# Performance work log

Hardware: AMD Instinct MI355X
Metric: run time of the kernel (lower is better)

## Reference

```python
import jax, jax.numpy as jnp
import numpy as np

B, N, F, F1 = 1024, 75, 512, 256
NEG = -1.0e9
ALPHA = 0.2  # LeakyReLU slope


def setup_inputs() -> dict:
    key = jax.random.key(0)
    k1, k2, k3, k4 = jax.random.split(key, 4)
    X = jax.random.normal(k1, (B, N, F), dtype=jnp.float32)
    A = jax.random.randint(k2, (N, N), 0, 2, dtype=jnp.int32)  # binary adjacency
    W = jax.random.normal(k3, (F, F1), dtype=jnp.float32) * (1.0 / np.sqrt(F))
    a = jax.random.normal(k4, (2, F1, 1), dtype=jnp.float32) * (1.0 / np.sqrt(F1))
    return {"X": X, "A": A, "W": W, "a": a}


def reference(X, A, W, a):
    # Linear projection: [B, N, F1]
    h = jnp.einsum('bnf,fo->bno', X, W)
    # Additive attention logits
    att_self = jnp.einsum('bno,od->bnd', h, a[0])        # [B, N, 1]
    att_neigh = jnp.einsum('bno,od->bnd', h, a[1])       # [B, N, 1]
    e = att_self + jnp.swapaxes(att_neigh, 1, 2)         # [B, N, N]
    e = jax.nn.leaky_relu(e, ALPHA)
    # Adjacency mask: disallowed edges get large negative bias
    adj = A.astype(h.dtype)                               # [N, N]
    e = e + NEG * (1.0 - adj)[None, :, :]
    # Normalize over neighbors, aggregate
    alpha = jax.nn.softmax(e, axis=-1)                    # [B, N, N]
    out = jnp.einsum('bij,bjo->bio', alpha, h)            # [B, N, F1]
    return jnp.concatenate([out, h], axis=-1)             # [B, N, 2*F1]
```

## Files before the change

### kernel.cpp

```cpp
#include <hip/hip_runtime.h>
#include <hip/hip_bf16.h>
#include <math.h>

typedef __bf16 bf16_t;
typedef __bf16 bf16x4_t __attribute__((ext_vector_type(4)));
typedef __bf16 bf16x8 __attribute__((ext_vector_type(8)));
typedef float f32x4 __attribute__((ext_vector_type(4)));
typedef unsigned long long u64;

#define NB 1024
#define NN 75
#define KF 512
#define F1 256
#define HSTR 100
#define ASTR 100

__global__ __launch_bounds__(256) void wt_kernel(const float* __restrict__ W,
                                                 bf16_t* __restrict__ Wt) {
    __shared__ float tile[64][65];
    const int kb = blockIdx.x * 64;
    const int nb = blockIdx.y * 64;
    const int tc = threadIdx.x & 63;
    const int tr = threadIdx.x >> 6;
#pragma unroll
    for (int r = tr; r < 64; r += 4)
        tile[r][tc] = W[(size_t)(kb + r) * F1 + nb + tc];
    __syncthreads();
#pragma unroll
    for (int r = tr; r < 64; r += 4)
        Wt[(size_t)(nb + r) * KF + kb + tc] = (bf16_t)tile[tc][r];
}

__global__ __launch_bounds__(256) void gemm_kernel(const float* __restrict__ X,
                                                   const bf16_t* __restrict__ Wt,
                                                   float* __restrict__ out) {
    __shared__ __align__(16) bf16_t Xs[64 * 512];

    const int t = threadIdx.x;
    const int w = t >> 6;
    const int l = t & 63;
    const int lc = l & 15;
    const int lr = l >> 4;
    const int m0 = blockIdx.x * 64;

    const bf16_t* wp0 = Wt + (size_t)(w * 64 + 0 * 16 + lc) * KF + lr * 8;
    const bf16_t* wp1 = Wt + (size_t)(w * 64 + 1 * 16 + lc) * KF + lr * 8;
    const bf16_t* wp2 = Wt + (size_t)(w * 64 + 2 * 16 + lc) * KF + lr * 8;
    const bf16_t* wp3 = Wt + (size_t)(w * 64 + 3 * 16 + lc) * KF + lr * 8;

    bf16x8 wA[4], wB[4];
#define WLOAD(WREG, KS)                                        \
    WREG[0] = *(const bf16x8*)(wp0 + (KS) * 32);               \
    WREG[1] = *(const bf16x8*)(wp1 + (KS) * 32);               \
    WREG[2] = *(const bf16x8*)(wp2 + (KS) * 32);               \
    WREG[3] = *(const bf16x8*)(wp3 + (KS) * 32);

    WLOAD(wA, 0);

    const int xrow  = ((t >> 6) << 4) + (t & 15);
    const int kpart = ((t >> 4) & 3) * 8;
    const float* xsrc = X + (size_t)(m0 + xrow) * KF + kpart;
#pragma unroll
    for (int q = 0; q < 16; ++q) {
        const float4 xa = *(const float4*)(xsrc + q * 32);
        const float4 xb = *(const float4*)(xsrc + q * 32 + 4);
        bf16x8 v;
        v[0]=(bf16_t)xa.x; v[1]=(bf16_t)xa.y; v[2]=(bf16_t)xa.z; v[3]=(bf16_t)xa.w;
        v[4]=(bf16_t)xb.x; v[5]=(bf16_t)xb.y; v[6]=(bf16_t)xb.z; v[7]=(bf16_t)xb.w;
        *(bf16x8*)&Xs[(q * 256 + t) * 8] = v;
    }
    __syncthreads();

    f32x4 acc[4][4];
#pragma unroll
    for (int i = 0; i < 4; ++i)
#pragma unroll
        for (int j = 0; j < 4; ++j) acc[i][j] = (f32x4){0.f, 0.f, 0.f, 0.f};

#define GSTEP(KS, WREG)                                                        \
    {                                                                          \
        bf16x8 af[4];                                                          \
        _Pragma("unroll")                                                      \
        for (int mt = 0; mt < 4; ++mt)                                         \
            af[mt] = *(const bf16x8*)&Xs[((KS) * 256 + mt * 64 + l) * 8];      \
        _Pragma("unroll")                                                      \
        for (int mt = 0; mt < 4; ++mt)                                         \
            _Pragma("unroll")                                                  \
            for (int ntl = 0; ntl < 4; ++ntl)                                  \
                acc[mt][ntl] = __builtin_amdgcn_mfma_f32_16x16x32_bf16(        \
                    af[mt], WREG[ntl], acc[mt][ntl], 0, 0, 0);                 \
    }

#pragma unroll
    for (int kp = 0; kp < 8; ++kp) {
        const int ks0 = kp * 2;
        const int ks1 = kp * 2 + 1;
        WLOAD(wB, ks1);
        GSTEP(ks0, wA);
        if (ks1 < 15) { WLOAD(wA, ks1 + 1); }
        GSTEP(ks1, wB);
    }
#undef GSTEP
#undef WLOAD

#pragma unroll
    for (int mt = 0; mt < 4; ++mt) {
#pragma unroll
        for (int ntl = 0; ntl < 4; ++ntl) {
            const int col = w * 64 + ntl * 16 + lc;
#pragma unroll
            for (int j = 0; j < 4; ++j) {
                const int row = m0 + mt * 16 + lr * 4 + j;
                out[(size_t)row * 512 + 256 + col] = acc[mt][ntl][j];
            }
        }
    }
}

__global__ __launch_bounds__(256) void pv_kernel(const int* __restrict__ Adj,
                                                 const float* __restrict__ avec,
                                                 float* __restrict__ out) {
    __shared__ __align__(16) bf16_t hT[256 * HSTR];
    __shared__ __align__(16) bf16_t alp[80 * ASTR];
    __shared__ float a0s[F1], a1s[F1];
    __shared__ float attp0[4][80], attp1[4][80];
    __shared__ float att0s[80], att1s[80], rsums[80];
    __shared__ u64 adjb[160];

    const int b = blockIdx.x;
    const int t = threadIdx.x;
    const int w = t >> 6;
    const int l = t & 63;
    const int lc = l & 15;
    const int lr = l >> 4;
    float* outb = out + (size_t)b * NN * 512;

    a0s[t] = avec[t];
    a1s[t] = avec[F1 + t];
    for (int i = w; i < NN; i += 4) {
        const int v0 = Adj[i * NN + l];
        const int v1 = (l < NN - 64) ? Adj[i * NN + 64 + l] : 0;
        const u64 b0 = __ballot(v0 != 0);
        const u64 b1 = __ballot(v1 != 0);
        if (l == 0) { adjb[i * 2] = b0; adjb[i * 2 + 1] = b1; }
    }
    {
        int* z = (int*)&hT[t * HSTR + 80];
#pragma unroll
        for (int k = 0; k < 8; ++k) z[k] = 0;
    }
    __syncthreads();

    const int c0 = w * 64 + lc * 4;
    const float4 a04 = *(const float4*)&a0s[c0];
    const float4 a14 = *(const float4*)&a1s[c0];
#pragma unroll
    for (int jp = 0; jp < 5; ++jp) {
        const int j0 = jp * 16 + lr * 4;
        float hr[4][4];
#pragma unroll
        for (int r = 0; r < 4; ++r) {
            if (j0 + r < NN) {
                const float4 v = *(const float4*)(outb + (size_t)(j0 + r) * 512 + 256 + c0);
                hr[r][0] = v.x; hr[r][1] = v.y; hr[r][2] = v.z; hr[r][3] = v.w;
            } else {
                hr[r][0] = hr[r][1] = hr[r][2] = hr[r][3] = 0.f;
            }
        }
        float p0[4], p1[4];
#pragma unroll
        for (int r = 0; r < 4; ++r) {
            p0[r] = hr[r][0] * a04.x + hr[r][1] * a04.y + hr[r][2] * a04.z + hr[r][3] * a04.w;
            p1[r] = hr[r][0] * a14.x + hr[r][1] * a14.y + hr[r][2] * a14.z + hr[r][3] * a14.w;
        }
#pragma unroll
        for (int off = 1; off < 16; off <<= 1) {
#pragma unroll
            for (int r = 0; r < 4; ++r) {
                p0[r] += __shfl_xor(p0[r], off);
                p1[r] += __shfl_xor(p1[r], off);
            }
        }
        if (lc == 0) {
#pragma unroll
            for (int r = 0; r < 4; ++r) {
                attp0[w][j0 + r] = p0[r];
                attp1[w][j0 + r] = p1[r];
            }
        }
#pragma unroll
        for (int cc = 0; cc < 4; ++cc) {
            bf16x4_t v;
            v[0] = (bf16_t)hr[0][cc]; v[1] = (bf16_t)hr[1][cc];
            v[2] = (bf16_t)hr[2][cc]; v[3] = (bf16_t)hr[3][cc];
            *(bf16x4_t*)&hT[(c0 + cc) * HSTR + j0] = v;
        }
    }
    __syncthreads();

    if (t < 80)
        att0s[t] = attp0[0][t] + attp0[1][t] + attp0[2][t] + attp0[3][t];
    else if (t < 160)
        att1s[t - 80] = attp1[0][t - 80] + attp1[1][t - 80] + attp1[2][t - 80] + attp1[3][t - 80];
    else if (t < 240) {
        const int r = t - 160;
        if (r < NN) {
            for (int c = NN; c < 96; ++c) alp[r * ASTR + c] = (bf16_t)0.f;
        } else {
            for (int c = 0; c < 96; ++c) alp[r * ASTR + c] = (bf16_t)0.f;
        }
    }
    __syncthreads();

    {
        const int gid = t >> 2;
        const int k4 = t & 3;
#pragma unroll
        for (int r = 0; r < 2; ++r) {
            const int i = r * 64 + gid;
            if (i < NN) {
                const float a0i = att0s[i];
                const u64 w0 = adjb[i * 2];
                const u64 w1 = adjb[i * 2 + 1];
                float e[19];
                float m = -3.0e38f;
#pragma unroll
                for (int jj = 0; jj < 19; ++jj) {
                    const int j = jj * 4 + k4;
                    float ev = -3.0e38f;
                    if (j < NN) {
                        float x = a0i + att1s[j];
                        x = x > 0.f ? x : 0.2f * x;
                        const u64 wj = (j < 64) ? w0 : w1;
                        const int bit = (int)((wj >> (j & 63)) & 1);
                        ev = bit ? x : x - 1.0e9f;
                    }
                    e[jj] = ev;
                    m = fmaxf(m, ev);
                }
                m = fmaxf(m, __shfl_xor(m, 1));
                m = fmaxf(m, __shfl_xor(m, 2));
                float s = 0.f;
#pragma unroll
                for (int jj = 0; jj < 19; ++jj) {
                    const int j = jj * 4 + k4;
                    if (j < NN) {
                        const float ex = __expf(e[jj] - m);
                        s += ex;
                        alp[i * ASTR + j] = (bf16_t)ex;
                    }
                }
                s += __shfl_xor(s, 1);
                s += __shfl_xor(s, 2);
                if (k4 == 0) rsums[i] = 1.f / s;
            }
        }
    }
    __syncthreads();

    f32x4 acc2[5][4];
#pragma unroll
    for (int i = 0; i < 5; ++i)
#pragma unroll
        for (int j = 0; j < 4; ++j) acc2[i][j] = (f32x4){0.f, 0.f, 0.f, 0.f};

#pragma unroll
    for (int ks = 0; ks < 3; ++ks) {
        bf16x8 bv[4];
#pragma unroll
        for (int ntl = 0; ntl < 4; ++ntl) {
            const bf16_t* q = &hT[(w * 64 + ntl * 16 + lc) * HSTR + ks * 32 + lr * 8];
            ((uint2*)&bv[ntl])[0] = *(const uint2*)q;
            ((uint2*)&bv[ntl])[1] = *(const uint2*)(q + 4);
        }
#pragma unroll
        for (int mt = 0; mt < 5; ++mt) {
            const bf16_t* ap = &alp[(mt * 16 + lc) * ASTR + ks * 32 + lr * 8];
            bf16x8 av;
            ((uint2*)&av)[0] = *(const uint2*)ap;
            ((uint2*)&av)[1] = *(const uint2*)(ap + 4);
#pragma unroll
            for (int ntl = 0; ntl < 4; ++ntl)
                acc2[mt][ntl] = __builtin_amdgcn_mfma_f32_16x16x32_bf16(av, bv[ntl], acc2[mt][ntl], 0, 0, 0);
        }
    }

#pragma unroll
    for (int mt = 0; mt < 5; ++mt) {
#pragma unroll
        for (int j = 0; j < 4; ++j) {
            const int row = mt * 16 + lr * 4 + j;
            if (row < NN) {
                const float rsv = rsums[row];
#pragma unroll
                for (int ntl = 0; ntl < 4; ++ntl) {
                    const int ch = w * 64 + ntl * 16 + lc;
                    outb[(size_t)row * 512 + ch] = acc2[mt][ntl][j] * rsv;
                }
            }
        }
    }
}

extern "C" void kernel_launch(void* const* d_in, const int* in_sizes, int n_in,
                              void* d_out, int out_size, void* d_ws, size_t ws_size,
                              hipStream_t stream) {
    const float* X = (const float*)d_in[0];
    const int*   A = (const int*)d_in[1];
    const float* W = (const float*)d_in[2];
    const float* a = (const float*)d_in[3];
    float* out = (float*)d_out;
    bf16_t* Wt = (bf16_t*)d_ws;

    wt_kernel<<<dim3(KF / 64, F1 / 64), 256, 0, stream>>>(W, Wt);
    gemm_kernel<<<(NB * NN) / 64, 256, 0, stream>>>(X, Wt, out);
    pv_kernel<<<NB, 256, 0, stream>>>(A, a, out);
}
```

Baseline: 131.8 us.

## Double-buffer X tiles via global_load_lds with swizzled fp32 LDS layout

Replaces the up-front load of the whole 64x512 X tile (converted to bf16 into a 64 KB LDS buffer) with a two-stage pipeline. Each stage copies a 64-column fp32 slice directly into LDS with global_load_lds, using an XOR swizzle to avoid bank conflicts, and bf16 conversion moves to the point where fragments are read. The smaller 32 KB LDS footprint and a launch bound of 3 blocks per SM aim to raise occupancy and overlap global loads with MFMA work. In exchange there are eight extra barriers per block and the conversion is repeated per fragment read. There is also a risk that the async LDS load needs an explicit vmcnt wait before the barrier.

```diff
diff --git a/kernel.cpp b/kernel.cpp
--- a/kernel.cpp
+++ b/kernel.cpp
@@ -7,6 +7,9 @@
 typedef __bf16 bf16x8 __attribute__((ext_vector_type(8)));
 typedef float f32x4 __attribute__((ext_vector_type(4)));
 typedef unsigned long long u64;
+
+typedef __attribute__((address_space(1))) const unsigned int cu32_g;
+typedef __attribute__((address_space(3))) unsigned int u32_s;
 
 #define NB 1024
 #define NN 75
@@ -31,10 +34,10 @@
         Wt[(size_t)(nb + r) * KF + kb + tc] = (bf16_t)tile[tc][r];
 }
 
-__global__ __launch_bounds__(256) void gemm_kernel(const float* __restrict__ X,
-                                                   const bf16_t* __restrict__ Wt,
-                                                   float* __restrict__ out) {
-    __shared__ __align__(16) bf16_t Xs[64 * 512];
+__global__ __launch_bounds__(256, 3) void gemm_kernel(const float* __restrict__ X,
+                                                      const bf16_t* __restrict__ Wt,
+                                                      float* __restrict__ out) {
+    __shared__ __align__(16) float XsF[2 * 4096];
 
     const int t = threadIdx.x;
     const int w = t >> 6;
@@ -43,33 +46,30 @@
     const int lr = l >> 4;
     const int m0 = blockIdx.x * 64;
 
+    const int c_row = w * 4 + lr;
+    const int sd    = (l & 15) ^ (c_row & 7);
+    const float* gsrc = X + (size_t)(m0 + c_row) * KF + sd * 4;
+
+#define STAGE(BUF, KS64)                                                       \
+    {                                                                          \
+        _Pragma("unroll")                                                      \
+        for (int u = 0; u < 4; ++u) {                                          \
+            const float* g = gsrc + (size_t)u * 16 * KF + (KS64) * 64;         \
+            float* lp = XsF + (BUF) * 4096 + (u * 4 + w) * 256;                \
+            __builtin_amdgcn_global_load_lds((cu32_g*)g, (u32_s*)lp, 16, 0, 0);\
+        }                                                                      \
+    }
+
     const bf16_t* wp0 = Wt + (size_t)(w * 64 + 0 * 16 + lc) * KF + lr * 8;
     const bf16_t* wp1 = Wt + (size_t)(w * 64 + 1 * 16 + lc) * KF + lr * 8;
     const bf16_t* wp2 = Wt + (size_t)(w * 64 + 2 * 16 + lc) * KF + lr * 8;
     const bf16_t* wp3 = Wt + (size_t)(w * 64 + 3 * 16 + lc) * KF + lr * 8;
-
     bf16x8 wA[4], wB[4];
-#define WLOAD(WREG, KS)                                        \
-    WREG[0] = *(const bf16x8*)(wp0 + (KS) * 32);               \
-    WREG[1] = *(const bf16x8*)(wp1 + (KS) * 32);               \
-    WREG[2] = *(const bf16x8*)(wp2 + (KS) * 32);               \
-    WREG[3] = *(const bf16x8*)(wp3 + (KS) * 32);
-
-    WLOAD(wA, 0);
-
-    const int xrow  = ((t >> 6) << 4) + (t & 15);
-    const int kpart = ((t >> 4) & 3) * 8;
-    const float* xsrc = X + (size_t)(m0 + xrow) * KF + kpart;
-#pragma unroll
-    for (int q = 0; q < 16; ++q) {
-        const float4 xa = *(const float4*)(xsrc + q * 32);
-        const float4 xb = *(const float4*)(xsrc + q * 32 + 4);
-        bf16x8 v;
-        v[0]=(bf16_t)xa.x; v[1]=(bf16_t)xa.y; v[2]=(bf16_t)xa.z; v[3]=(bf16_t)xa.w;
-        v[4]=(bf16_t)xb.x; v[5]=(bf16_t)xb.y; v[6]=(bf16_t)xb.z; v[7]=(bf16_t)xb.w;
-        *(bf16x8*)&Xs[(q * 256 + t) * 8] = v;
-    }
-    __syncthreads();
+#define WLOAD(WREG, KS32)                                      \
+    WREG[0] = *(const bf16x8*)(wp0 + (KS32) * 32);             \
+    WREG[1] = *(const bf16x8*)(wp1 + (KS32) * 32);             \
+    WREG[2] = *(const bf16x8*)(wp2 + (KS32) * 32);             \
+    WREG[3] = *(const bf16x8*)(wp3 + (KS32) * 32);
 
     f32x4 acc[4][4];
 #pragma unroll
@@ -77,12 +77,23 @@
 #pragma unroll
         for (int j = 0; j < 4; ++j) acc[i][j] = (f32x4){0.f, 0.f, 0.f, 0.f};
 
-#define GSTEP(KS, WREG)                                                        \
+#define GSTEP32(BUF, KO, WREG)                                                 \
     {                                                                          \
         bf16x8 af[4];                                                          \
         _Pragma("unroll")                                                      \
-        for (int mt = 0; mt < 4; ++mt)                                         \
-            af[mt] = *(const bf16x8*)&Xs[((KS) * 256 + mt * 64 + l) * 8];      \
+        for (int mt = 0; mt < 4; ++mt) {                                       \
+            const int rowl = mt * 16 + lc;                                     \
+            const int xr = rowl & 7;                                           \
+            const int s0 = ((KO) >> 2) + lr * 2;                               \
+            const float4 fa = *(const float4*)&XsF[(BUF) * 4096 + rowl * 64 +  \
+                                                   ((s0 ^ xr) << 2)];          \
+            const float4 fb = *(const float4*)&XsF[(BUF) * 4096 + rowl * 64 +  \
+                                                   (((s0 + 1) ^ xr) << 2)];    \
+            af[mt][0] = (bf16_t)fa.x; af[mt][1] = (bf16_t)fa.y;                \
+            af[mt][2] = (bf16_t)fa.z; af[mt][3] = (bf16_t)fa.w;                \
+            af[mt][4] = (bf16_t)fb.x; af[mt][5] = (bf16_t)fb.y;                \
+            af[mt][6] = (bf16_t)fb.z; af[mt][7] = (bf16_t)fb.w;                \
+        }                                                                      \
         _Pragma("unroll")                                                      \
         for (int mt = 0; mt < 4; ++mt)                                         \
             _Pragma("unroll")                                                  \
@@ -91,17 +102,24 @@
                     af[mt], WREG[ntl], acc[mt][ntl], 0, 0, 0);                 \
     }
 
-#pragma unroll
-    for (int kp = 0; kp < 8; ++kp) {
-        const int ks0 = kp * 2;
-        const int ks1 = kp * 2 + 1;
-        WLOAD(wB, ks1);
-        GSTEP(ks0, wA);
-        if (ks1 < 15) { WLOAD(wA, ks1 + 1); }
-        GSTEP(ks1, wB);
-    }
-#undef GSTEP
+    WLOAD(wA, 0);
+    STAGE(0, 0);
+    __syncthreads();
+
+    int buf = 0;
+#pragma unroll
+    for (int ks64 = 0; ks64 < 8; ++ks64) {
+        if (ks64 < 7) STAGE(buf ^ 1, ks64 + 1);
+        WLOAD(wB, 2 * ks64 + 1);
+        GSTEP32(buf, 0, wA);
+        if (2 * ks64 + 2 < 16) { WLOAD(wA, 2 * ks64 + 2); }
+        GSTEP32(buf, 32, wB);
+        __syncthreads();
+        buf ^= 1;
+    }
+#undef GSTEP32
 #undef WLOAD
+#undef STAGE
 
 #pragma unroll
     for (int mt = 0; mt < 4; ++mt) {
```

After: 131.7 us. About the same (-0.1%).

## Pipeline GEMM X tiles via async global_load_lds with multi-stage ring buffer

Applied to the files above, without the earlier changes.

Replaces the upfront load-and-convert of the whole 64x512 X block into LDS with a 6-slot ring buffer filled by async global_load_lds (fp32, XOR-swizzled), issued four k-steps ahead together with register-prefetched W fragments. Each iteration waits on vmcnt, barriers, converts fp32 to bf16 from LDS, and runs the MFMAs. The LDS footprint drops from 64KB to 48KB and launch bounds request 2 blocks per CU, aiming to overlap memory with compute and raise occupancy. The cost is per-iteration barriers, fp32-to-bf16 conversion inside the loop, hand-tuned vmcnt counts that must match the issued loads exactly, and more W registers held live.

```diff
diff --git a/kernel.cpp b/kernel.cpp
--- a/kernel.cpp
+++ b/kernel.cpp
@@ -7,6 +7,9 @@
 typedef __bf16 bf16x8 __attribute__((ext_vector_type(8)));
 typedef float f32x4 __attribute__((ext_vector_type(4)));
 typedef unsigned long long u64;
+
+typedef __attribute__((address_space(1))) const unsigned int cu32_g;
+typedef __attribute__((address_space(3))) unsigned int u32_s;
 
 #define NB 1024
 #define NN 75
@@ -31,10 +34,10 @@
         Wt[(size_t)(nb + r) * KF + kb + tc] = (bf16_t)tile[tc][r];
 }
 
-__global__ __launch_bounds__(256) void gemm_kernel(const float* __restrict__ X,
-                                                   const bf16_t* __restrict__ Wt,
-                                                   float* __restrict__ out) {
-    __shared__ __align__(16) bf16_t Xs[64 * 512];
+__global__ __launch_bounds__(256, 2) void gemm_kernel(const float* __restrict__ X,
+                                                      const bf16_t* __restrict__ Wt,
+                                                      float* __restrict__ out) {
+    __shared__ __align__(16) float XsF[6 * 2048];
 
     const int t = threadIdx.x;
     const int w = t >> 6;
@@ -43,65 +46,72 @@
     const int lr = l >> 4;
     const int m0 = blockIdx.x * 64;
 
-    const bf16_t* wp0 = Wt + (size_t)(w * 64 + 0 * 16 + lc) * KF + lr * 8;
-    const bf16_t* wp1 = Wt + (size_t)(w * 64 + 1 * 16 + lc) * KF + lr * 8;
-    const bf16_t* wp2 = Wt + (size_t)(w * 64 + 2 * 16 + lc) * KF + lr * 8;
-    const bf16_t* wp3 = Wt + (size_t)(w * 64 + 3 * 16 + lc) * KF + lr * 8;
-
-    bf16x8 wA[4], wB[4];
-#define WLOAD(WREG, KS)                                        \
-    WREG[0] = *(const bf16x8*)(wp0 + (KS) * 32);               \
-    WREG[1] = *(const bf16x8*)(wp1 + (KS) * 32);               \
-    WREG[2] = *(const bf16x8*)(wp2 + (KS) * 32);               \
-    WREG[3] = *(const bf16x8*)(wp3 + (KS) * 32);
-
-    WLOAD(wA, 0);
-
-    const int xrow  = ((t >> 6) << 4) + (t & 15);
-    const int kpart = ((t >> 4) & 3) * 8;
-    const float* xsrc = X + (size_t)(m0 + xrow) * KF + kpart;
-#pragma unroll
-    for (int q = 0; q < 16; ++q) {
-        const float4 xa = *(const float4*)(xsrc + q * 32);
-        const float4 xb = *(const float4*)(xsrc + q * 32 + 4);
-        bf16x8 v;
-        v[0]=(bf16_t)xa.x; v[1]=(bf16_t)xa.y; v[2]=(bf16_t)xa.z; v[3]=(bf16_t)xa.w;
-        v[4]=(bf16_t)xb.x; v[5]=(bf16_t)xb.y; v[6]=(bf16_t)xb.z; v[7]=(bf16_t)xb.w;
-        *(bf16x8*)&Xs[(q * 256 + t) * 8] = v;
-    }
-    __syncthreads();
-
+    const float* Xg = X + (size_t)(m0 + w * 8 + (l >> 3)) * KF
+                        + (((l & 7) ^ (l >> 3)) << 2);
+
+    const bf16_t* wp0 = Wt + (size_t)(w * 64 +  0 + lc) * KF + lr * 8;
+    const bf16_t* wp1 = Wt + (size_t)(w * 64 + 16 + lc) * KF + lr * 8;
+    const bf16_t* wp2 = Wt + (size_t)(w * 64 + 32 + lc) * KF + lr * 8;
+    const bf16_t* wp3 = Wt + (size_t)(w * 64 + 48 + lc) * KF + lr * 8;
+
+    bf16x8 wg[4][4];
     f32x4 acc[4][4];
 #pragma unroll
     for (int i = 0; i < 4; ++i)
 #pragma unroll
         for (int j = 0; j < 4; ++j) acc[i][j] = (f32x4){0.f, 0.f, 0.f, 0.f};
 
-#define GSTEP(KS, WREG)                                                        \
+#define ISSUE(SLOT)                                                            \
+    if ((SLOT) < 16) {                                                         \
+        _Pragma("unroll")                                                      \
+        for (int u = 0; u < 2; ++u) {                                          \
+            const float* g = Xg + (size_t)u * 32 * KF + (SLOT) * 32;           \
+            float* lp = XsF + ((SLOT) % 6) * 2048 + (u * 256 + w * 64) * 4;    \
+            __builtin_amdgcn_global_load_lds((cu32_g*)g, (u32_s*)lp, 16, 0, 0);\
+        }                                                                      \
+        wg[(SLOT) % 4][0] = *(const bf16x8*)(wp0 + (SLOT) * 32);               \
+        wg[(SLOT) % 4][1] = *(const bf16x8*)(wp1 + (SLOT) * 32);               \
+        wg[(SLOT) % 4][2] = *(const bf16x8*)(wp2 + (SLOT) * 32);               \
+        wg[(SLOT) % 4][3] = *(const bf16x8*)(wp3 + (SLOT) * 32);               \
+    }                                                                          \
+    __builtin_amdgcn_sched_barrier(0);
+
+#define ITER(I, NWAIT)                                                         \
     {                                                                          \
-        bf16x8 af[4];                                                          \
+        asm volatile("s_waitcnt vmcnt(" #NWAIT ")" ::: "memory");              \
+        __builtin_amdgcn_s_barrier();                                          \
+        __builtin_amdgcn_sched_barrier(0);                                     \
         _Pragma("unroll")                                                      \
-        for (int mt = 0; mt < 4; ++mt)                                         \
-            af[mt] = *(const bf16x8*)&Xs[((KS) * 256 + mt * 64 + l) * 8];      \
-        _Pragma("unroll")                                                      \
-        for (int mt = 0; mt < 4; ++mt)                                         \
+        for (int mt = 0; mt < 4; ++mt) {                                       \
+            const int row = mt * 16 + lc;                                      \
+            const int x7 = lc & 7;                                             \
+            const float4 fa = *(const float4*)&XsF[((I) % 6) * 2048 +          \
+                row * 32 + (((lr * 2) ^ x7) << 2)];                            \
+            const float4 fb = *(const float4*)&XsF[((I) % 6) * 2048 +          \
+                row * 32 + (((lr * 2 + 1) ^ x7) << 2)];                        \
+            bf16x8 af;                                                         \
+            af[0] = (bf16_t)fa.x; af[1] = (bf16_t)fa.y;                        \
+            af[2] = (bf16_t)fa.z; af[3] = (bf16_t)fa.w;                        \
+            af[4] = (bf16_t)fb.x; af[5] = (bf16_t)fb.y;                        \
+            af[6] = (bf16_t)fb.z; af[7] = (bf16_t)fb.w;                        \
             _Pragma("unroll")                                                  \
             for (int ntl = 0; ntl < 4; ++ntl)                                  \
                 acc[mt][ntl] = __builtin_amdgcn_mfma_f32_16x16x32_bf16(        \
-                    af[mt], WREG[ntl], acc[mt][ntl], 0, 0, 0);                 \
-    }
-
-#pragma unroll
-    for (int kp = 0; kp < 8; ++kp) {
-        const int ks0 = kp * 2;
-        const int ks1 = kp * 2 + 1;
-        WLOAD(wB, ks1);
-        GSTEP(ks0, wA);
-        if (ks1 < 15) { WLOAD(wA, ks1 + 1); }
-        GSTEP(ks1, wB);
-    }
-#undef GSTEP
-#undef WLOAD
+                    af, wg[(I) % 4][ntl], acc[mt][ntl], 0, 0, 0);              \
+        }                                                                      \
+        __builtin_amdgcn_sched_barrier(0);                                     \
+        ISSUE((I) + 4);                                                        \
+    }
+
+    ISSUE(0); ISSUE(1); ISSUE(2); ISSUE(3);
+
+    ITER(0, 18)  ITER(1, 18)  ITER(2, 18)  ITER(3, 18)
+    ITER(4, 18)  ITER(5, 18)  ITER(6, 18)  ITER(7, 18)
+    ITER(8, 18)  ITER(9, 18)  ITER(10, 18) ITER(11, 18)
+    ITER(12, 18) ITER(13, 12) ITER(14, 6)  ITER(15, 0)
+
+#undef ITER
+#undef ISSUE
 
 #pragma unroll
     for (int mt = 0; mt < 4; ++mt) {
```

Measured after the change: 140.1 us. +6.2%, slower.
